# Optimization experiments

Measured on AMD Instinct MI355X. Metric: run time of the kernel, lower is better.

The kernel has to match this reference:

```python
import jax, jax.numpy as jnp
import numpy as np
from jax import lax

B, L = 2, 1024
D_MODEL, D_STATE, EXPAND, D_CONV = 1024, 16, 2, 4
D_INNER = EXPAND * D_MODEL            # 2048
DT_RANK = (D_MODEL + 15) // 16        # 64


def setup_inputs() -> dict:
    key = jax.random.key(0)
    ks = jax.random.split(key, 8)
    g = lambda k, shape, s=0.02: jax.random.normal(k, shape, dtype=jnp.float32) * s
    # Mamba-style A init: A = -exp(A_log), A_log = log(1..d_state) per channel
    A_log = jnp.log(jnp.broadcast_to(
        jnp.arange(1, D_STATE + 1, dtype=jnp.float32), (D_INNER, D_STATE)))
    return {
        "x": jax.random.normal(ks[0], (B, L, D_MODEL), dtype=jnp.float32),
        "W_in": g(ks[1], (D_MODEL, 2 * D_INNER)),
        "conv_w": g(ks[2], (D_INNER, D_CONV), 0.1),
        "conv_b": jnp.zeros((D_INNER,), jnp.float32),
        "W_x": g(ks[3], (D_INNER, DT_RANK + 2 * D_STATE)),
        "W_dt": g(ks[4], (DT_RANK, D_INNER)),
        "b_dt": g(ks[5], (D_INNER,), 0.1),
        "A_log": A_log,
        "D_skip": jnp.ones((D_INNER,), jnp.float32),
        "W_out": g(ks[6], (D_INNER, D_MODEL)),
    }


def reference(x, W_in, conv_w, conv_b, W_x, W_dt, b_dt, A_log, D_skip, W_out):
    # in_proj -> (u, z): [B, L, D_INNER] each
    xz = x @ W_in
    u, z = xz[..., :D_INNER], xz[..., D_INNER:]

    # causal depthwise conv1d, kernel D_CONV (small fixed loop over taps)
    up = jnp.pad(u, ((0, 0), (D_CONV - 1, 0), (0, 0)))
    u = sum(up[:, k:k + L, :] * conv_w[:, k] for k in range(D_CONV)) + conv_b
    u = jax.nn.silu(u)

    # input-dependent dt, B, C
    x_dbl = u @ W_x                                    # [B, L, dt_rank + 2N]
    dt = x_dbl[..., :DT_RANK]
    Bm = x_dbl[..., DT_RANK:DT_RANK + D_STATE]         # [B, L, N]
    Cm = x_dbl[..., DT_RANK + D_STATE:]                # [B, L, N]
    delta = jax.nn.softplus(dt @ W_dt + b_dt)          # [B, L, D]

    A = -jnp.exp(A_log)                                # [D, N]
    deltaA = jnp.exp(jnp.einsum('bld,dn->bldn', delta, A))   # [B, L, D, N]
    dBu = (delta * u)[..., None] * Bm[:, :, None, :]          # [B, L, D, N]

    def step(h, inp):
        dA_t, dBu_t, c_t = inp                         # [B,D,N],[B,D,N],[B,N]
        h = dA_t * h + dBu_t
        y_t = jnp.einsum('bdn,bn->bd', h, c_t)
        return h, y_t

    h0 = jnp.zeros((B, D_INNER, D_STATE), x.dtype)
    _, ys = lax.scan(step, h0,
                     (deltaA.transpose(1, 0, 2, 3),
                      dBu.transpose(1, 0, 2, 3),
                      Cm.transpose(1, 0, 2)))
    y = ys.transpose(1, 0, 2) + u * D_skip             # [B, L, D_INNER]
    y = y * jax.nn.silu(z)                             # gated output
    return y @ W_out                                   # [B, L, D_MODEL]
```

## Files before the change

kernel.cpp:

```cpp
#include <hip/hip_runtime.h>


typedef unsigned short u16;
typedef unsigned int   u32;

#define B_SZ 2
#define L_SZ 1024
#define DM   1024
#define DI   2048
#define DS   16
#define DTR  64
#define NXD  96
#define NCHUNK 32
#define CL   32
#define KSPLIT 8
#define KC     256

typedef __bf16 bf16x8 __attribute__((ext_vector_type(8)));
typedef float  f32x4  __attribute__((ext_vector_type(4)));

__device__ __forceinline__ u16 f2bf(float f) {
    u32 x = __float_as_uint(f);
    x += 0x7fffu + ((x >> 16) & 1u);
    return (u16)(x >> 16);
}
__device__ __forceinline__ float bf2f(u16 v) {
    return __uint_as_float(((u32)v) << 16);
}

__device__ __forceinline__ void gld_lds16(const u16* g, u16* l) {
    __builtin_amdgcn_global_load_lds(
        (const __attribute__((address_space(1))) u32*)g,
        (__attribute__((address_space(3))) u32*)l, 16, 0, 0);
}

__device__ __forceinline__ void wg_barrier() {
    __asm__ volatile("" ::: "memory");
    __builtin_amdgcn_s_barrier();
    __asm__ volatile("" ::: "memory");
}
#define WAIT_VM12() __builtin_amdgcn_s_waitcnt(0xF7C)
#define WAIT_VM9()  __builtin_amdgcn_s_waitcnt(0xF79)
#define WAIT_VM8()  __builtin_amdgcn_s_waitcnt(0xF78)
#define WAIT_VM6()  __builtin_amdgcn_s_waitcnt(0xF76)
#define WAIT_VM4()  __builtin_amdgcn_s_waitcnt(0xF74)
#define WAIT_VM3()  __builtin_amdgcn_s_waitcnt(0xF73)
#define WAIT_VM0()  __builtin_amdgcn_s_waitcnt(0xF70)

__global__ __launch_bounds__(256) void gemm128p(
    const u16* __restrict__ A, const u16* __restrict__ BT,
    float* __restrict__ Cf, u16* __restrict__ Cb,
    int M, int N, int K, int op)
{
    __shared__ u16 As[4][128 * 32];
    __shared__ u16 Bs[4][128 * 32];

    const int tid  = threadIdx.x;
    const int wave = tid >> 6;
    const int lane = tid & 63;
    const int q    = lane >> 4;
    const int r16  = lane & 15;
    const int wm   = (wave & 1) * 64;
    const int wn   = (wave >> 1) * 64;
    const int m0   = blockIdx.y * 128;
    const int n0   = blockIdx.x * 128;

    const u16* gA0 = A  + (size_t)(m0 + (tid >> 2))      * K + (tid & 3) * 8;
    const u16* gA1 = A  + (size_t)(m0 + 64 + (tid >> 2)) * K + (tid & 3) * 8;
    const u16* gB0 = BT + (size_t)(n0 + (tid >> 2))      * K + (tid & 3) * 8;
    const u16* gB1 = BT + (size_t)(n0 + 64 + (tid >> 2)) * K + (tid & 3) * 8;

    const int niter = K >> 5;
    const int pre = niter < 3 ? niter : 3;
    for (int p = 0; p < pre; ++p) {
        const int k0 = p * 32;
        gld_lds16(gA0 + k0, &As[p][tid * 8]);
        gld_lds16(gA1 + k0, &As[p][2048 + tid * 8]);
        gld_lds16(gB0 + k0, &Bs[p][tid * 8]);
        gld_lds16(gB1 + k0, &Bs[p][2048 + tid * 8]);
    }

    f32x4 acc[4][4];
#pragma unroll
    for (int s = 0; s < 4; ++s)
#pragma unroll
        for (int j = 0; j < 4; ++j) acc[s][j] = (f32x4){0.f, 0.f, 0.f, 0.f};

    for (int it = 0; it < niter; ++it) {
        if (it + 3 < niter) {
            const int k0 = (it + 3) * 32;
            const int bi = (it + 3) & 3;
            gld_lds16(gA0 + k0, &As[bi][tid * 8]);
            gld_lds16(gA1 + k0, &As[bi][2048 + tid * 8]);
            gld_lds16(gB0 + k0, &Bs[bi][tid * 8]);
            gld_lds16(gB1 + k0, &Bs[bi][2048 + tid * 8]);
            WAIT_VM12();
        } else if (it + 2 < niter) {
            WAIT_VM8();
        } else if (it + 1 < niter) {
            WAIT_VM4();
        } else {
            WAIT_VM0();
        }
        wg_barrier();

        const int cur = it & 3;
        bf16x8 af[4], bfr[4];
#pragma unroll
        for (int s = 0; s < 4; ++s)
            af[s] = *(const bf16x8*)(&As[cur][(wm + s * 16 + r16) * 32 + q * 8]);
#pragma unroll
        for (int j = 0; j < 4; ++j)
            bfr[j] = *(const bf16x8*)(&Bs[cur][(wn + j * 16 + r16) * 32 + q * 8]);
#pragma unroll
        for (int s = 0; s < 4; ++s)
#pragma unroll
            for (int j = 0; j < 4; ++j)
                acc[s][j] = __builtin_amdgcn_mfma_f32_16x16x32_bf16(
                    af[s], bfr[j], acc[s][j], 0, 0, 0);

        wg_barrier();
    }

#pragma unroll
    for (int s = 0; s < 4; ++s) {
        const int row0 = m0 + wm + s * 16 + q * 4;
#pragma unroll
        for (int j = 0; j < 4; ++j) {
            const int col = n0 + wn + j * 16 + r16;
            if (op == 2) {
#pragma unroll
                for (int i = 0; i < 4; ++i)
                    Cb[(size_t)(row0 + i) * N + col] = f2bf(acc[s][j][i]);
            } else {
#pragma unroll
                for (int i = 0; i < 4; ++i)
                    Cf[(size_t)(row0 + i) * N + col] = acc[s][j][i];
            }
        }
    }
}

__global__ __launch_bounds__(256) void gemm_out64(
    const u16* __restrict__ A, const u16* __restrict__ BT,
    float* __restrict__ C, int M, int N, int K)
{
    __shared__ u16 As[4][128 * 32];
    __shared__ u16 Bs[4][64 * 32];

    const int tid  = threadIdx.x;
    const int wave = tid >> 6;
    const int lane = tid & 63;
    const int q    = lane >> 4;
    const int r16  = lane & 15;
    const int wm   = (wave & 1) * 64;
    const int wn   = (wave >> 1) * 32;
    const int m0   = blockIdx.y * 128;
    const int n0   = blockIdx.x * 64;

    const u16* gA0 = A  + (size_t)(m0 + (tid >> 2))      * K + (tid & 3) * 8;
    const u16* gA1 = A  + (size_t)(m0 + 64 + (tid >> 2)) * K + (tid & 3) * 8;
    const u16* gB0 = BT + (size_t)(n0 + (tid >> 2))      * K + (tid & 3) * 8;

    const int niter = K >> 5;
    const int pre = niter < 3 ? niter : 3;
    for (int p = 0; p < pre; ++p) {
        const int k0 = p * 32;
        gld_lds16(gA0 + k0, &As[p][tid * 8]);
        gld_lds16(gA1 + k0, &As[p][2048 + tid * 8]);
        gld_lds16(gB0 + k0, &Bs[p][tid * 8]);
    }

    f32x4 acc[4][2];
#pragma unroll
    for (int s = 0; s < 4; ++s)
#pragma unroll
        for (int j = 0; j < 2; ++j) acc[s][j] = (f32x4){0.f, 0.f, 0.f, 0.f};

    for (int it = 0; it < niter; ++it) {
        if (it + 3 < niter) {
            const int k0 = (it + 3) * 32;
            const int bi = (it + 3) & 3;
            gld_lds16(gA0 + k0, &As[bi][tid * 8]);
            gld_lds16(gA1 + k0, &As[bi][2048 + tid * 8]);
            gld_lds16(gB0 + k0, &Bs[bi][tid * 8]);
            WAIT_VM9();
        } else if (it + 2 < niter) {
            WAIT_VM6();
        } else if (it + 1 < niter) {
            WAIT_VM3();
        } else {
            WAIT_VM0();
        }
        wg_barrier();

        const int cur = it & 3;
        bf16x8 af[4], bfr[2];
#pragma unroll
        for (int s = 0; s < 4; ++s)
            af[s] = *(const bf16x8*)(&As[cur][(wm + s * 16 + r16) * 32 + q * 8]);
#pragma unroll
        for (int j = 0; j < 2; ++j)
            bfr[j] = *(const bf16x8*)(&Bs[cur][(wn + j * 16 + r16) * 32 + q * 8]);
#pragma unroll
        for (int s = 0; s < 4; ++s)
#pragma unroll
            for (int j = 0; j < 2; ++j)
                acc[s][j] = __builtin_amdgcn_mfma_f32_16x16x32_bf16(
                    af[s], bfr[j], acc[s][j], 0, 0, 0);

        wg_barrier();
    }

#pragma unroll
    for (int s = 0; s < 4; ++s) {
        const int row0 = m0 + wm + s * 16 + q * 4;
#pragma unroll
        for (int j = 0; j < 2; ++j) {
            const int col = n0 + wn + j * 16 + r16;
#pragma unroll
            for (int i = 0; i < 4; ++i)
                C[(size_t)(row0 + i) * N + col] = acc[s][j][i];
        }
    }
}

__global__ __launch_bounds__(256) void gemm_skinny_atomic(
    const u16* __restrict__ A, const u16* __restrict__ BT,
    float* xdbl, int M, int N, int K)
{
    constexpr int LDT = 40;
    __shared__ u16 As[128 * LDT];
    __shared__ u16 Bs[64 * LDT];

    const int tid  = threadIdx.x;
    const int wave = tid >> 6;
    const int lane = tid & 63;
    const int q    = lane >> 4;
    const int r16  = lane & 15;
    const int m0   = blockIdx.y * 128;
    const int n0   = blockIdx.x * 64;
    const int kcs  = blockIdx.z * KC;
    const int sr   = tid >> 2;
    const int ss   = (tid & 3) * 8;

    f32x4 acc[2][4];
#pragma unroll
    for (int s = 0; s < 2; ++s)
#pragma unroll
        for (int j = 0; j < 4; ++j) acc[s][j] = (f32x4){0.f, 0.f, 0.f, 0.f};

    const int bcol  = n0 + sr;
    const int bcolc = bcol < N ? bcol : N - 1;

    constexpr int NIT = KC / 32;
    uint4 a0 = *(const uint4*)(A + (size_t)(m0 + sr)      * K + kcs + ss);
    uint4 a1 = *(const uint4*)(A + (size_t)(m0 + 64 + sr) * K + kcs + ss);
    uint4 bv = *(const uint4*)(BT + (size_t)bcolc * K + kcs + ss);

    for (int it = 0; it < NIT; ++it) {
        wg_barrier();
        *(uint4*)(As + sr * LDT + ss)        = a0;
        *(uint4*)(As + (64 + sr) * LDT + ss) = a1;
        *(uint4*)(Bs + sr * LDT + ss)        = bv;
        const int kn = (it + 1 < NIT) ? (kcs + (it + 1) * 32) : kcs;
        a0 = *(const uint4*)(A + (size_t)(m0 + sr)      * K + kn + ss);
        a1 = *(const uint4*)(A + (size_t)(m0 + 64 + sr) * K + kn + ss);
        bv = *(const uint4*)(BT + (size_t)bcolc * K + kn + ss);
        __builtin_amdgcn_s_waitcnt(0xF70 | 0x0000);
        __builtin_amdgcn_s_waitcnt(0x070F);
        wg_barrier();

        bf16x8 af[2], bfr[4];
#pragma unroll
        for (int s = 0; s < 2; ++s)
            af[s] = *(const bf16x8*)(As + (wave * 32 + s * 16 + r16) * LDT + q * 8);
#pragma unroll
        for (int j = 0; j < 4; ++j)
            bfr[j] = *(const bf16x8*)(Bs + (j * 16 + r16) * LDT + q * 8);
#pragma unroll
        for (int s = 0; s < 2; ++s)
#pragma unroll
            for (int j = 0; j < 4; ++j)
                acc[s][j] = __builtin_amdgcn_mfma_f32_16x16x32_bf16(
                    af[s], bfr[j], acc[s][j], 0, 0, 0);
    }

#pragma unroll
    for (int s = 0; s < 2; ++s) {
        const int row0 = m0 + wave * 32 + s * 16 + q * 4;
#pragma unroll
        for (int j = 0; j < 4; ++j) {
            const int col = n0 + j * 16 + r16;
            if (col < N) {
#pragma unroll
                for (int i = 0; i < 4; ++i)
                    atomicAdd(&xdbl[(size_t)(row0 + i) * N + col], acc[s][j][i]);
            }
        }
    }
}

__global__ __launch_bounds__(256) void gemm_delta(
    const float* __restrict__ xdbl, const u16* __restrict__ BT,
    const float* __restrict__ bias, float* __restrict__ dlt)
{
    constexpr int LDT = 40;
    __shared__ u16 As[128 * LDT];
    __shared__ u16 Bs[128 * LDT];

    const int tid  = threadIdx.x;
    const int wave = tid >> 6;
    const int lane = tid & 63;
    const int q    = lane >> 4;
    const int r16  = lane & 15;
    const int wm   = (wave & 1) * 64;
    const int wn   = (wave >> 1) * 64;
    const int m0   = blockIdx.y * 128;
    const int n0   = blockIdx.x * 128;
    const int sr   = tid >> 2;
    const int ss   = (tid & 3) * 8;

    f32x4 acc[4][4];
#pragma unroll
    for (int s = 0; s < 4; ++s)
#pragma unroll
        for (int j = 0; j < 4; ++j) acc[s][j] = (f32x4){0.f, 0.f, 0.f, 0.f};

    for (int k0 = 0; k0 < DTR; k0 += 32) {
        __syncthreads();
        f32x4 f0 = *(const f32x4*)(xdbl + (size_t)(m0 + sr) * NXD + k0 + ss);
        f32x4 f1 = *(const f32x4*)(xdbl + (size_t)(m0 + sr) * NXD + k0 + ss + 4);
        f32x4 f2 = *(const f32x4*)(xdbl + (size_t)(m0 + 64 + sr) * NXD + k0 + ss);
        f32x4 f3 = *(const f32x4*)(xdbl + (size_t)(m0 + 64 + sr) * NXD + k0 + ss + 4);
        uint4 bv0 = *(const uint4*)(BT + (size_t)(n0 + sr)      * DTR + k0 + ss);
        uint4 bv1 = *(const uint4*)(BT + (size_t)(n0 + 64 + sr) * DTR + k0 + ss);
        u16* pa0 = As + sr * LDT + ss;
        u16* pa1 = As + (64 + sr) * LDT + ss;
#pragma unroll
        for (int i = 0; i < 4; ++i) { pa0[i] = f2bf(f0[i]); pa0[4 + i] = f2bf(f1[i]); }
#pragma unroll
        for (int i = 0; i < 4; ++i) { pa1[i] = f2bf(f2[i]); pa1[4 + i] = f2bf(f3[i]); }
        *(uint4*)(Bs + sr * LDT + ss)        = bv0;
        *(uint4*)(Bs + (64 + sr) * LDT + ss) = bv1;
        __syncthreads();

        bf16x8 af[4], bfr[4];
#pragma unroll
        for (int s = 0; s < 4; ++s)
            af[s] = *(const bf16x8*)(As + (wm + s * 16 + r16) * LDT + q * 8);
#pragma unroll
        for (int j = 0; j < 4; ++j)
            bfr[j] = *(const bf16x8*)(Bs + (wn + j * 16 + r16) * LDT + q * 8);
#pragma unroll
        for (int s = 0; s < 4; ++s)
#pragma unroll
            for (int j = 0; j < 4; ++j)
                acc[s][j] = __builtin_amdgcn_mfma_f32_16x16x32_bf16(
                    af[s], bfr[j], acc[s][j], 0, 0, 0);
    }

#pragma unroll
    for (int s = 0; s < 4; ++s) {
        const int row0 = m0 + wm + s * 16 + q * 4;
#pragma unroll
        for (int j = 0; j < 4; ++j) {
            const int col = n0 + wn + j * 16 + r16;
            const float bv = bias[col];
#pragma unroll
            for (int i = 0; i < 4; ++i) {
                float v = acc[s][j][i] + bv;
                v = (v > 20.f) ? v : log1pf(__expf(v));
                dlt[(size_t)(row0 + i) * DI + col] = v;
            }
        }
    }
}

__device__ __forceinline__ void tr_tile(
    const float* __restrict__ in, u16* __restrict__ out,
    int R, int C, int tr, int tc, int tid, float (*t)[33])
{
    const int tx = tid & 31, ty = tid >> 5;
    const int r0 = tr * 32, c0 = tc * 32;
#pragma unroll
    for (int i = 0; i < 4; ++i) {
        int r = r0 + ty + i * 8, c = c0 + tx;
        if (r < R && c < C) t[ty + i * 8][tx] = in[(size_t)r * C + c];
    }
    __syncthreads();
#pragma unroll
    for (int i = 0; i < 4; ++i) {
        int oR = c0 + ty + i * 8, oC = r0 + tx;
        if (oR < C && oC < R) out[(size_t)oR * R + oC] = f2bf(t[tx][ty + i * 8]);
    }
}

__global__ __launch_bounds__(256) void prep_kernel(
    const float* __restrict__ x,     u16* __restrict__ xbf,
    const float* __restrict__ W_in,  u16* __restrict__ winT,
    const float* __restrict__ W_out, u16* __restrict__ woutT,
    const float* __restrict__ W_x,   u16* __restrict__ wxT,
    const float* __restrict__ W_dt,  u16* __restrict__ wdtT,
    float* __restrict__ xdbl)
{
    __shared__ float t[32][33];
    const int id  = blockIdx.x;
    const int tid = threadIdx.x;
    if (id < 4096) {
        tr_tile(W_in, winT, 1024, 4096, id >> 7, id & 127, tid, t);
    } else if (id < 6144) {
        int i2 = id - 4096;
        tr_tile(W_out, woutT, 2048, 1024, i2 >> 5, i2 & 31, tid, t);
    } else if (id < 6336) {
        int i3 = id - 6144;
        tr_tile(W_x, wxT, 2048, 96, i3 / 3, i3 % 3, tid, t);
    } else if (id < 6464) {
        int i4 = id - 6336;
        tr_tile(W_dt, wdtT, 64, 2048, i4 >> 6, i4 & 63, tid, t);
    } else if (id < 14656) {
        int i = (id - 6464) * 256 + tid;
        xbf[i] = f2bf(x[i]);
    } else {
        f32x4 z = (f32x4){0.f, 0.f, 0.f, 0.f};
        ((f32x4*)xdbl)[(size_t)(id - 14656) * 256 + tid] = z;
    }
}

__global__ __launch_bounds__(256) void conv_silu_kernel(
    const u16* __restrict__ xzbf, const float* __restrict__ cw,
    const float* __restrict__ cb, u16* __restrict__ ucbf)
{
    const int idx = blockIdx.x * 256 + threadIdx.x;
    const int d   = idx & (DI - 1);
    const int pos = idx >> 11;
    const int l   = pos & (L_SZ - 1);
    float s = cb[d];
#pragma unroll
    for (int k = 0; k < 4; ++k) {
        int ls = l + k - 3;
        if (ls >= 0)
            s = fmaf(bf2f(xzbf[(size_t)(pos + k - 3) * (2 * DI) + d]), cw[d * 4 + k], s);
    }
    float v = s / (1.f + __expf(-s));
    ucbf[idx] = f2bf(v);
}

__global__ __launch_bounds__(256) void scan_pass1(
    const float* __restrict__ delta, const u16* __restrict__ ucbf,
    const float* __restrict__ xdbl, const float* __restrict__ A_log,
    float* __restrict__ hbuf, float* __restrict__ pbuf)
{
    const int c = blockIdx.x;
    const int d = blockIdx.y * 256 + threadIdx.x;
    const int b = blockIdx.z;
    float Av[16], h[16], P[16];
#pragma unroll
    for (int n = 0; n < 16; ++n) {
        Av[n] = -__expf(A_log[d * 16 + n]);
        h[n] = 0.f; P[n] = 1.f;
    }
    const int rowbase = b * L_SZ + c * CL;
    for (int i = 0; i < CL; ++i) {
        const int row = rowbase + i;
        float dlt = delta[(size_t)row * DI + d];
        float uu  = bf2f(ucbf[(size_t)row * DI + d]);
        float du  = dlt * uu;
        const float* xr = xdbl + (size_t)row * NXD;
#pragma unroll
        for (int n = 0; n < 16; ++n) {
            float e = __expf(dlt * Av[n]);
            P[n] *= e;
            h[n] = fmaf(e, h[n], du * xr[DTR + n]);
        }
    }
    size_t base = ((size_t)((b * NCHUNK + c) * DI + d)) * 16;
#pragma unroll
    for (int n = 0; n < 16; ++n) { hbuf[base + n] = h[n]; pbuf[base + n] = P[n]; }
}

__global__ __launch_bounds__(256) void scan_pass2(
    float* __restrict__ hbuf, const float* __restrict__ pbuf)
{
    const int j = blockIdx.x * 256 + threadIdx.x;
    const int b = blockIdx.y;
    float h0 = 0.f;
    for (int cc = 0; cc < NCHUNK; ++cc) {
        size_t o = ((size_t)(b * NCHUNK + cc)) * (DI * 16) + j;
        float hl = hbuf[o];
        float Pl = pbuf[o];
        hbuf[o] = h0;
        h0 = fmaf(Pl, h0, hl);
    }
}

__global__ __launch_bounds__(256) void scan_pass3(
    const float* __restrict__ delta, const u16* __restrict__ ucbf,
    const float* __restrict__ xdbl, const float* __restrict__ A_log,
    const float* __restrict__ hbuf, const u16* __restrict__ xzbf,
    const float* __restrict__ Dskip, u16* __restrict__ ybf)
{
    const int c = blockIdx.x;
    const int d = blockIdx.y * 256 + threadIdx.x;
    const int b = blockIdx.z;
    float Av[16], h[16];
    size_t base = ((size_t)((b * NCHUNK + c) * DI + d)) * 16;
#pragma unroll
    for (int n = 0; n < 16; ++n) {
        Av[n] = -__expf(A_log[d * 16 + n]);
        h[n]  = hbuf[base + n];
    }
    const float Dk = Dskip[d];
    const int rowbase = b * L_SZ + c * CL;
    for (int i = 0; i < CL; ++i) {
        const int row = rowbase + i;
        float dlt = delta[(size_t)row * DI + d];
        float uu  = bf2f(ucbf[(size_t)row * DI + d]);
        float du  = dlt * uu;
        const float* xr = xdbl + (size_t)row * NXD;
        float y = 0.f;
#pragma unroll
        for (int n = 0; n < 16; ++n) {
            float e = __expf(dlt * Av[n]);
            h[n] = fmaf(e, h[n], du * xr[DTR + n]);
            y = fmaf(h[n], xr[DTR + DS + n], y);
        }
        float zz = bf2f(xzbf[(size_t)row * (2 * DI) + DI + d]);
        float yv = fmaf(uu, Dk, y) * (zz / (1.f + __expf(-zz)));
        ybf[(size_t)row * DI + d] = f2bf(yv);
    }
}

constexpr size_t OFF_DELTA   = 0;
constexpr size_t OFF_XDBL    = OFF_DELTA + 4194304;
constexpr size_t OFF_HBUF    = OFF_XDBL  + 196608;
constexpr size_t OFF_PBUF    = OFF_HBUF  + 2097152;
constexpr size_t OFF_F32_END = OFF_PBUF  + 2097152;
constexpr size_t SOFF_XBF   = 0;
constexpr size_t SOFF_WINT  = SOFF_XBF   + 2097152;
constexpr size_t SOFF_XZBF  = SOFF_WINT  + 4194304;
constexpr size_t SOFF_UCBF  = SOFF_XZBF  + 8388608;
constexpr size_t SOFF_WXT   = SOFF_UCBF  + 4194304;
constexpr size_t SOFF_WDTT  = SOFF_WXT   + 196608;
constexpr size_t SOFF_WOUTT = SOFF_WDTT  + 131072;
constexpr size_t SOFF_YBF   = SOFF_WOUTT + 2097152;

extern "C" void kernel_launch(void* const* d_in, const int* in_sizes, int n_in,
                              void* d_out, int out_size, void* d_ws, size_t ws_size,
                              hipStream_t stream)
{
    const float* x     = (const float*)d_in[0];
    const float* W_in  = (const float*)d_in[1];
    const float* cw    = (const float*)d_in[2];
    const float* cb    = (const float*)d_in[3];
    const float* W_x   = (const float*)d_in[4];
    const float* W_dt  = (const float*)d_in[5];
    const float* b_dt  = (const float*)d_in[6];
    const float* A_log = (const float*)d_in[7];
    const float* Dsk   = (const float*)d_in[8];
    const float* W_out = (const float*)d_in[9];
    float* out = (float*)d_out;

    float* wsf   = (float*)d_ws;
    float* dlt   = wsf + OFF_DELTA;
    float* xdbl  = wsf + OFF_XDBL;
    float* hbuf  = wsf + OFF_HBUF;
    float* pbuf  = wsf + OFF_PBUF;
    u16* sb    = (u16*)(wsf + OFF_F32_END);
    u16* xbf   = sb + SOFF_XBF;
    u16* winT  = sb + SOFF_WINT;
    u16* xzbf  = sb + SOFF_XZBF;
    u16* ucbf  = sb + SOFF_UCBF;
    u16* wxT   = sb + SOFF_WXT;
    u16* wdtT  = sb + SOFF_WDTT;
    u16* woutT = sb + SOFF_WOUTT;
    u16* ybf   = sb + SOFF_YBF;

    prep_kernel<<<14848, 256, 0, stream>>>(x, xbf, W_in, winT, W_out, woutT,
                                           W_x, wxT, W_dt, wdtT, xdbl);

    gemm128p<<<dim3(32, 16), 256, 0, stream>>>(
        xbf, winT, nullptr, xzbf, 2048, 4096, 1024, 2);

    conv_silu_kernel<<<(B_SZ * L_SZ * DI) / 256, 256, 0, stream>>>(xzbf, cw, cb, ucbf);

    gemm_skinny_atomic<<<dim3(2, 16, KSPLIT), 256, 0, stream>>>(
        ucbf, wxT, xdbl, 2048, NXD, 2048);

    gemm_delta<<<dim3(16, 16), 256, 0, stream>>>(xdbl, wdtT, b_dt, dlt);

    scan_pass1<<<dim3(NCHUNK, DI / 256, B_SZ), 256, 0, stream>>>(dlt, ucbf, xdbl, A_log, hbuf, pbuf);
    scan_pass2<<<dim3(DI * 16 / 256, B_SZ), 256, 0, stream>>>(hbuf, pbuf);
    scan_pass3<<<dim3(NCHUNK, DI / 256, B_SZ), 256, 0, stream>>>(dlt, ucbf, xdbl, A_log, hbuf, xzbf, Dsk, ybf);

    gemm_out64<<<dim3(16, 16), 256, 0, stream>>>(ybf, woutT, out, 2048, 1024, 2048);
}
```

Measured before the change: 261.8 us.

## Fuse conv, x_proj, delta GEMM and scan passes into cooperative persistent kernel

After: 801.2 us. 3.06x slower.

```diff
diff --git a/kernel.cpp b/kernel.cpp
--- a/kernel.cpp
+++ b/kernel.cpp
@@ -1,4 +1,7 @@
 #include <hip/hip_runtime.h>
+#include <hip/hip_cooperative_groups.h>
+
+namespace cg = cooperative_groups;
 
 
 typedef unsigned short u16;
@@ -267,7 +270,6 @@
         a0 = *(const uint4*)(A + (size_t)(m0 + sr)      * K + kn + ss);
         a1 = *(const uint4*)(A + (size_t)(m0 + 64 + sr) * K + kn + ss);
         bv = *(const uint4*)(BT + (size_t)bcolc * K + kn + ss);
-        __builtin_amdgcn_s_waitcnt(0xF70 | 0x0000);
         __builtin_amdgcn_s_waitcnt(0x070F);
         wg_barrier();
 
@@ -373,6 +375,369 @@
                 v = (v > 20.f) ? v : log1pf(__expf(v));
                 dlt[(size_t)(row0 + i) * DI + col] = v;
             }
+        }
+    }
+}
+
+__global__ __launch_bounds__(256) void conv_silu_kernel(
+    const u16* __restrict__ xzbf, const float* __restrict__ cw,
+    const float* __restrict__ cb, u16* __restrict__ ucbf)
+{
+    const int idx = blockIdx.x * 256 + threadIdx.x;
+    const int d   = idx & (DI - 1);
+    const int pos = idx >> 11;
+    const int l   = pos & (L_SZ - 1);
+    float s = cb[d];
+#pragma unroll
+    for (int k = 0; k < 4; ++k) {
+        int ls = l + k - 3;
+        if (ls >= 0)
+            s = fmaf(bf2f(xzbf[(size_t)(pos + k - 3) * (2 * DI) + d]), cw[d * 4 + k], s);
+    }
+    float v = s / (1.f + __expf(-s));
+    ucbf[idx] = f2bf(v);
+}
+
+__global__ __launch_bounds__(256) void scan_pass1(
+    const float* __restrict__ delta, const u16* __restrict__ ucbf,
+    const float* __restrict__ xdbl, const float* __restrict__ A_log,
+    float* __restrict__ hbuf, float* __restrict__ pbuf)
+{
+    const int c = blockIdx.x;
+    const int d = blockIdx.y * 256 + threadIdx.x;
+    const int b = blockIdx.z;
+    float Av[16], h[16], P[16];
+#pragma unroll
+    for (int n = 0; n < 16; ++n) {
+        Av[n] = -__expf(A_log[d * 16 + n]);
+        h[n] = 0.f; P[n] = 1.f;
+    }
+    const int rowbase = b * L_SZ + c * CL;
+    for (int i = 0; i < CL; ++i) {
+        const int row = rowbase + i;
+        float dlt = delta[(size_t)row * DI + d];
+        float uu  = bf2f(ucbf[(size_t)row * DI + d]);
+        float du  = dlt * uu;
+        const float* xr = xdbl + (size_t)row * NXD;
+#pragma unroll
+        for (int n = 0; n < 16; ++n) {
+            float e = __expf(dlt * Av[n]);
+            P[n] *= e;
+            h[n] = fmaf(e, h[n], du * xr[DTR + n]);
+        }
+    }
+    size_t base = ((size_t)((b * NCHUNK + c) * DI + d)) * 16;
+#pragma unroll
+    for (int n = 0; n < 16; ++n) { hbuf[base + n] = h[n]; pbuf[base + n] = P[n]; }
+}
+
+__global__ __launch_bounds__(256) void scan_pass2(
+    float* __restrict__ hbuf, const float* __restrict__ pbuf)
+{
+    const int j = blockIdx.x * 256 + threadIdx.x;
+    const int b = blockIdx.y;
+    float h0 = 0.f;
+    for (int cc = 0; cc < NCHUNK; ++cc) {
+        size_t o = ((size_t)(b * NCHUNK + cc)) * (DI * 16) + j;
+        float hl = hbuf[o];
+        float Pl = pbuf[o];
+        hbuf[o] = h0;
+        h0 = fmaf(Pl, h0, hl);
+    }
+}
+
+__global__ __launch_bounds__(256) void scan_pass3(
+    const float* __restrict__ delta, const u16* __restrict__ ucbf,
+    const float* __restrict__ xdbl, const float* __restrict__ A_log,
+    const float* __restrict__ hbuf, const u16* __restrict__ xzbf,
+    const float* __restrict__ Dskip, u16* __restrict__ ybf)
+{
+    const int c = blockIdx.x;
+    const int d = blockIdx.y * 256 + threadIdx.x;
+    const int b = blockIdx.z;
+    float Av[16], h[16];
+    size_t base = ((size_t)((b * NCHUNK + c) * DI + d)) * 16;
+#pragma unroll
+    for (int n = 0; n < 16; ++n) {
+        Av[n] = -__expf(A_log[d * 16 + n]);
+        h[n]  = hbuf[base + n];
+    }
+    const float Dk = Dskip[d];
+    const int rowbase = b * L_SZ + c * CL;
+    for (int i = 0; i < CL; ++i) {
+        const int row = rowbase + i;
+        float dlt = delta[(size_t)row * DI + d];
+        float uu  = bf2f(ucbf[(size_t)row * DI + d]);
+        float du  = dlt * uu;
+        const float* xr = xdbl + (size_t)row * NXD;
+        float y = 0.f;
+#pragma unroll
+        for (int n = 0; n < 16; ++n) {
+            float e = __expf(dlt * Av[n]);
+            h[n] = fmaf(e, h[n], du * xr[DTR + n]);
+            y = fmaf(h[n], xr[DTR + DS + n], y);
+        }
+        float zz = bf2f(xzbf[(size_t)row * (2 * DI) + DI + d]);
+        float yv = fmaf(uu, Dk, y) * (zz / (1.f + __expf(-zz)));
+        ybf[(size_t)row * DI + d] = f2bf(yv);
+    }
+}
+
+#define MEGA_BLOCKS 512
+#define MEGA_THREADS_TOTAL (MEGA_BLOCKS * 256)
+
+__global__ __launch_bounds__(256, 2) void mega_kernel(
+    const u16* __restrict__ xzbf, const float* __restrict__ cw,
+    const float* __restrict__ cb, u16* __restrict__ ucbf,
+    const u16* __restrict__ wxT, float* __restrict__ xdbl,
+    const u16* __restrict__ wdtT, const float* __restrict__ b_dt,
+    float* __restrict__ dlt, const float* __restrict__ A_log,
+    float* __restrict__ hbuf, float* __restrict__ pbuf,
+    const float* __restrict__ Dsk, u16* __restrict__ ybf)
+{
+    constexpr int LDT = 40;
+    __shared__ u16 sA[128 * LDT];
+    __shared__ u16 sB[64 * LDT];
+
+    cg::grid_group grid = cg::this_grid();
+
+    const int blk = blockIdx.x;
+    const int tid = threadIdx.x;
+    const int wave = tid >> 6;
+    const int lane = tid & 63;
+    const int q    = lane >> 4;
+    const int r16  = lane & 15;
+
+    {
+        for (int idx = blk * 256 + tid; idx < B_SZ * L_SZ * DI;
+             idx += MEGA_THREADS_TOTAL) {
+            const int d   = idx & (DI - 1);
+            const int pos = idx >> 11;
+            const int l   = pos & (L_SZ - 1);
+            float s = cb[d];
+#pragma unroll
+            for (int k = 0; k < 4; ++k) {
+                int ls = l + k - 3;
+                if (ls >= 0)
+                    s = fmaf(bf2f(xzbf[(size_t)(pos + k - 3) * (2 * DI) + d]),
+                             cw[d * 4 + k], s);
+            }
+            float v = s / (1.f + __expf(-s));
+            ucbf[idx] = f2bf(v);
+        }
+    }
+    __threadfence();
+    grid.sync();
+
+    if (blk < 2 * 16 * KSPLIT) {
+        const int n0  = (blk & 1) * 64;
+        const int m0  = ((blk >> 1) & 15) * 128;
+        const int kcs = (blk >> 5) * KC;
+        const int sr  = tid >> 2;
+        const int ss  = (tid & 3) * 8;
+        const int K   = DI;
+        const int N   = NXD;
+
+        f32x4 acc[2][4];
+#pragma unroll
+        for (int s = 0; s < 2; ++s)
+#pragma unroll
+            for (int j = 0; j < 4; ++j) acc[s][j] = (f32x4){0.f, 0.f, 0.f, 0.f};
+
+        const int bcol  = n0 + sr;
+        const int bcolc = bcol < N ? bcol : N - 1;
+
+        constexpr int NIT = KC / 32;
+        uint4 a0 = *(const uint4*)(ucbf + (size_t)(m0 + sr)      * K + kcs + ss);
+        uint4 a1 = *(const uint4*)(ucbf + (size_t)(m0 + 64 + sr) * K + kcs + ss);
+        uint4 bv = *(const uint4*)(wxT + (size_t)bcolc * K + kcs + ss);
+
+        for (int it = 0; it < NIT; ++it) {
+            wg_barrier();
+            *(uint4*)(sA + sr * LDT + ss)        = a0;
+            *(uint4*)(sA + (64 + sr) * LDT + ss) = a1;
+            *(uint4*)(sB + sr * LDT + ss)        = bv;
+            const int kn = (it + 1 < NIT) ? (kcs + (it + 1) * 32) : kcs;
+            a0 = *(const uint4*)(ucbf + (size_t)(m0 + sr)      * K + kn + ss);
+            a1 = *(const uint4*)(ucbf + (size_t)(m0 + 64 + sr) * K + kn + ss);
+            bv = *(const uint4*)(wxT + (size_t)bcolc * K + kn + ss);
+            __builtin_amdgcn_s_waitcnt(0x070F);
+            wg_barrier();
+
+            bf16x8 af[2], bfr[4];
+#pragma unroll
+            for (int s = 0; s < 2; ++s)
+                af[s] = *(const bf16x8*)(sA + (wave * 32 + s * 16 + r16) * LDT + q * 8);
+#pragma unroll
+            for (int j = 0; j < 4; ++j)
+                bfr[j] = *(const bf16x8*)(sB + (j * 16 + r16) * LDT + q * 8);
+#pragma unroll
+            for (int s = 0; s < 2; ++s)
+#pragma unroll
+                for (int j = 0; j < 4; ++j)
+                    acc[s][j] = __builtin_amdgcn_mfma_f32_16x16x32_bf16(
+                        af[s], bfr[j], acc[s][j], 0, 0, 0);
+        }
+
+#pragma unroll
+        for (int s = 0; s < 2; ++s) {
+            const int row0 = m0 + wave * 32 + s * 16 + q * 4;
+#pragma unroll
+            for (int j = 0; j < 4; ++j) {
+                const int col = n0 + j * 16 + r16;
+                if (col < N) {
+#pragma unroll
+                    for (int i = 0; i < 4; ++i)
+                        atomicAdd(&xdbl[(size_t)(row0 + i) * N + col], acc[s][j][i]);
+                }
+            }
+        }
+    }
+    __threadfence();
+    grid.sync();
+
+    {
+        const int n0 = (blk & 31) * 64;
+        const int m0 = (blk >> 5) * 128;
+        const int wm = (wave & 1) * 64;
+        const int wn = (wave >> 1) * 32;
+        const int sr = tid >> 2;
+        const int ss = (tid & 3) * 8;
+
+        f32x4 acc[4][2];
+#pragma unroll
+        for (int s = 0; s < 4; ++s)
+#pragma unroll
+            for (int j = 0; j < 2; ++j) acc[s][j] = (f32x4){0.f, 0.f, 0.f, 0.f};
+
+        for (int k0 = 0; k0 < DTR; k0 += 32) {
+            __syncthreads();
+            f32x4 f0 = *(const f32x4*)(xdbl + (size_t)(m0 + sr) * NXD + k0 + ss);
+            f32x4 f1 = *(const f32x4*)(xdbl + (size_t)(m0 + sr) * NXD + k0 + ss + 4);
+            f32x4 f2 = *(const f32x4*)(xdbl + (size_t)(m0 + 64 + sr) * NXD + k0 + ss);
+            f32x4 f3 = *(const f32x4*)(xdbl + (size_t)(m0 + 64 + sr) * NXD + k0 + ss + 4);
+            uint4 bv0 = *(const uint4*)(wdtT + (size_t)(n0 + sr) * DTR + k0 + ss);
+            u16* pa0 = sA + sr * LDT + ss;
+            u16* pa1 = sA + (64 + sr) * LDT + ss;
+#pragma unroll
+            for (int i = 0; i < 4; ++i) { pa0[i] = f2bf(f0[i]); pa0[4 + i] = f2bf(f1[i]); }
+#pragma unroll
+            for (int i = 0; i < 4; ++i) { pa1[i] = f2bf(f2[i]); pa1[4 + i] = f2bf(f3[i]); }
+            *(uint4*)(sB + sr * LDT + ss) = bv0;
+            __syncthreads();
+
+            bf16x8 af[4], bfr[2];
+#pragma unroll
+            for (int s = 0; s < 4; ++s)
+                af[s] = *(const bf16x8*)(sA + (wm + s * 16 + r16) * LDT + q * 8);
+#pragma unroll
+            for (int j = 0; j < 2; ++j)
+                bfr[j] = *(const bf16x8*)(sB + (wn + j * 16 + r16) * LDT + q * 8);
+#pragma unroll
+            for (int s = 0; s < 4; ++s)
+#pragma unroll
+                for (int j = 0; j < 2; ++j)
+                    acc[s][j] = __builtin_amdgcn_mfma_f32_16x16x32_bf16(
+                        af[s], bfr[j], acc[s][j], 0, 0, 0);
+        }
+
+#pragma unroll
+        for (int s = 0; s < 4; ++s) {
+            const int row0 = m0 + wm + s * 16 + q * 4;
+#pragma unroll
+            for (int j = 0; j < 2; ++j) {
+                const int col = n0 + wn + j * 16 + r16;
+                const float bv = b_dt[col];
+#pragma unroll
+                for (int i = 0; i < 4; ++i) {
+                    float v = acc[s][j][i] + bv;
+                    v = (v > 20.f) ? v : log1pf(__expf(v));
+                    dlt[(size_t)(row0 + i) * DI + col] = v;
+                }
+            }
+        }
+    }
+    __threadfence();
+    grid.sync();
+
+    {
+        const int c = blk & 31;
+        const int d = ((blk >> 5) & 7) * 256 + tid;
+        const int b = blk >> 8;
+        float Av[16], h[16], P[16];
+#pragma unroll
+        for (int n = 0; n < 16; ++n) {
+            Av[n] = -__expf(A_log[d * 16 + n]);
+            h[n] = 0.f; P[n] = 1.f;
+        }
+        const int rowbase = b * L_SZ + c * CL;
+        for (int i = 0; i < CL; ++i) {
+            const int row = rowbase + i;
+            float dl = dlt[(size_t)row * DI + d];
+            float uu = bf2f(ucbf[(size_t)row * DI + d]);
+            float du = dl * uu;
+            const float* xr = xdbl + (size_t)row * NXD;
+#pragma unroll
+            for (int n = 0; n < 16; ++n) {
+                float e = __expf(dl * Av[n]);
+                P[n] *= e;
+                h[n] = fmaf(e, h[n], du * xr[DTR + n]);
+            }
+        }
+        size_t base = ((size_t)((b * NCHUNK + c) * DI + d)) * 16;
+#pragma unroll
+        for (int n = 0; n < 16; ++n) { hbuf[base + n] = h[n]; pbuf[base + n] = P[n]; }
+    }
+    __threadfence();
+    grid.sync();
+
+    {
+        const int idx = blk * 256 + tid;
+        if (idx < B_SZ * DI * 16) {
+            const int b = idx >> 15;
+            const int j = idx & (DI * 16 - 1);
+            float h0 = 0.f;
+            for (int cc = 0; cc < NCHUNK; ++cc) {
+                size_t o = ((size_t)(b * NCHUNK + cc)) * (DI * 16) + j;
+                float hl = hbuf[o];
+                float Pl = pbuf[o];
+                hbuf[o] = h0;
+                h0 = fmaf(Pl, h0, hl);
+            }
+        }
+    }
+    __threadfence();
+    grid.sync();
+
+    {
+        const int c = blk & 31;
+        const int d = ((blk >> 5) & 7) * 256 + tid;
+        const int b = blk >> 8;
+        float Av[16], h[16];
+        size_t base = ((size_t)((b * NCHUNK + c) * DI + d)) * 16;
+#pragma unroll
+        for (int n = 0; n < 16; ++n) {
+            Av[n] = -__expf(A_log[d * 16 + n]);
+            h[n]  = hbuf[base + n];
+        }
+        const float Dk = Dsk[d];
+        const int rowbase = b * L_SZ + c * CL;
+        for (int i = 0; i < CL; ++i) {
+            const int row = rowbase + i;
+            float dl = dlt[(size_t)row * DI + d];
+            float uu = bf2f(ucbf[(size_t)row * DI + d]);
+            float du = dl * uu;
+            const float* xr = xdbl + (size_t)row * NXD;
+            float y = 0.f;
+#pragma unroll
+            for (int n = 0; n < 16; ++n) {
+                float e = __expf(dl * Av[n]);
+                h[n] = fmaf(e, h[n], du * xr[DTR + n]);
+                y = fmaf(h[n], xr[DTR + DS + n], y);
+            }
+            float zz = bf2f(xzbf[(size_t)row * (2 * DI) + DI + d]);
+            float yv = fmaf(uu, Dk, y) * (zz / (1.f + __expf(-zz)));
+            ybf[(size_t)row * DI + d] = f2bf(yv);
         }
     }
 }
@@ -427,110 +792,6 @@
     }
 }
 
-__global__ __launch_bounds__(256) void conv_silu_kernel(
-    const u16* __restrict__ xzbf, const float* __restrict__ cw,
-    const float* __restrict__ cb, u16* __restrict__ ucbf)
-{
-    const int idx = blockIdx.x * 256 + threadIdx.x;
-    const int d   = idx & (DI - 1);
-    const int pos = idx >> 11;
-    const int l   = pos & (L_SZ - 1);
-    float s = cb[d];
-#pragma unroll
-    for (int k = 0; k < 4; ++k) {
-        int ls = l + k - 3;
-        if (ls >= 0)
-            s = fmaf(bf2f(xzbf[(size_t)(pos + k - 3) * (2 * DI) + d]), cw[d * 4 + k], s);
-    }
-    float v = s / (1.f + __expf(-s));
-    ucbf[idx] = f2bf(v);
-}
-
-__global__ __launch_bounds__(256) void scan_pass1(
-    const float* __restrict__ delta, const u16* __restrict__ ucbf,
-    const float* __restrict__ xdbl, const float* __restrict__ A_log,
-    float* __restrict__ hbuf, float* __restrict__ pbuf)
-{
-    const int c = blockIdx.x;
-    const int d = blockIdx.y * 256 + threadIdx.x;
-    const int b = blockIdx.z;
-    float Av[16], h[16], P[16];
-#pragma unroll
-    for (int n = 0; n < 16; ++n) {
-        Av[n] = -__expf(A_log[d * 16 + n]);
-        h[n] = 0.f; P[n] = 1.f;
-    }
-    const int rowbase = b * L_SZ + c * CL;
-    for (int i = 0; i < CL; ++i) {
-        const int row = rowbase + i;
-        float dlt = delta[(size_t)row * DI + d];
-        float uu  = bf2f(ucbf[(size_t)row * DI + d]);
-        float du  = dlt * uu;
-        const float* xr = xdbl + (size_t)row * NXD;
-#pragma unroll
-        for (int n = 0; n < 16; ++n) {
-            float e = __expf(dlt * Av[n]);
-            P[n] *= e;
-            h[n] = fmaf(e, h[n], du * xr[DTR + n]);
-        }
-    }
-    size_t base = ((size_t)((b * NCHUNK + c) * DI + d)) * 16;
-#pragma unroll
-    for (int n = 0; n < 16; ++n) { hbuf[base + n] = h[n]; pbuf[base + n] = P[n]; }
-}
-
-__global__ __launch_bounds__(256) void scan_pass2(
-    float* __restrict__ hbuf, const float* __restrict__ pbuf)
-{
-    const int j = blockIdx.x * 256 + threadIdx.x;
-    const int b = blockIdx.y;
-    float h0 = 0.f;
-    for (int cc = 0; cc < NCHUNK; ++cc) {
-        size_t o = ((size_t)(b * NCHUNK + cc)) * (DI * 16) + j;
-        float hl = hbuf[o];
-        float Pl = pbuf[o];
-        hbuf[o] = h0;
-        h0 = fmaf(Pl, h0, hl);
-    }
-}
-
-__global__ __launch_bounds__(256) void scan_pass3(
-    const float* __restrict__ delta, const u16* __restrict__ ucbf,
-    const float* __restrict__ xdbl, const float* __restrict__ A_log,
-    const float* __restrict__ hbuf, const u16* __restrict__ xzbf,
-    const float* __restrict__ Dskip, u16* __restrict__ ybf)
-{
-    const int c = blockIdx.x;
-    const int d = blockIdx.y * 256 + threadIdx.x;
-    const int b = blockIdx.z;
-    float Av[16], h[16];
-    size_t base = ((size_t)((b * NCHUNK + c) * DI + d)) * 16;
-#pragma unroll
-    for (int n = 0; n < 16; ++n) {
-        Av[n] = -__expf(A_log[d * 16 + n]);
-        h[n]  = hbuf[base + n];
-    }
-    const float Dk = Dskip[d];
-    const int rowbase = b * L_SZ + c * CL;
-    for (int i = 0; i < CL; ++i) {
-        const int row = rowbase + i;
-        float dlt = delta[(size_t)row * DI + d];
-        float uu  = bf2f(ucbf[(size_t)row * DI + d]);
-        float du  = dlt * uu;
-        const float* xr = xdbl + (size_t)row * NXD;
-        float y = 0.f;
-#pragma unroll
-        for (int n = 0; n < 16; ++n) {
-            float e = __expf(dlt * Av[n]);
-            h[n] = fmaf(e, h[n], du * xr[DTR + n]);
-            y = fmaf(h[n], xr[DTR + DS + n], y);
-        }
-        float zz = bf2f(xzbf[(size_t)row * (2 * DI) + DI + d]);
-        float yv = fmaf(uu, Dk, y) * (zz / (1.f + __expf(-zz)));
-        ybf[(size_t)row * DI + d] = f2bf(yv);
-    }
-}
-
 constexpr size_t OFF_DELTA   = 0;
 constexpr size_t OFF_XDBL    = OFF_DELTA + 4194304;
 constexpr size_t OFF_HBUF    = OFF_XDBL  + 196608;
@@ -582,16 +843,29 @@
     gemm128p<<<dim3(32, 16), 256, 0, stream>>>(
         xbf, winT, nullptr, xzbf, 2048, 4096, 1024, 2);
 
-    conv_silu_kernel<<<(B_SZ * L_SZ * DI) / 256, 256, 0, stream>>>(xzbf, cw, cb, ucbf);
-
-    gemm_skinny_atomic<<<dim3(2, 16, KSPLIT), 256, 0, stream>>>(
-        ucbf, wxT, xdbl, 2048, NXD, 2048);
-
-    gemm_delta<<<dim3(16, 16), 256, 0, stream>>>(xdbl, wdtT, b_dt, dlt);
-
-    scan_pass1<<<dim3(NCHUNK, DI / 256, B_SZ), 256, 0, stream>>>(dlt, ucbf, xdbl, A_log, hbuf, pbuf);
-    scan_pass2<<<dim3(DI * 16 / 256, B_SZ), 256, 0, stream>>>(hbuf, pbuf);
-    scan_pass3<<<dim3(NCHUNK, DI / 256, B_SZ), 256, 0, stream>>>(dlt, ucbf, xdbl, A_log, hbuf, xzbf, Dsk, ybf);
+    {
+        void* kargs[] = {
+            (void*)&xzbf, (void*)&cw, (void*)&cb, (void*)&ucbf,
+            (void*)&wxT, (void*)&xdbl, (void*)&wdtT, (void*)&b_dt,
+            (void*)&dlt, (void*)&A_log, (void*)&hbuf, (void*)&pbuf,
+            (void*)&Dsk, (void*)&ybf
+        };
+        hipError_t ce = hipLaunchCooperativeKernel(
+            (const void*)mega_kernel, dim3(MEGA_BLOCKS), dim3(256),
+            kargs, 0, stream);
+        if (ce != hipSuccess) {
+            conv_silu_kernel<<<(B_SZ * L_SZ * DI) / 256, 256, 0, stream>>>(
+                xzbf, cw, cb, ucbf);
+            gemm_skinny_atomic<<<dim3(2, 16, KSPLIT), 256, 0, stream>>>(
+                ucbf, wxT, xdbl, 2048, NXD, 2048);
+            gemm_delta<<<dim3(16, 16), 256, 0, stream>>>(xdbl, wdtT, b_dt, dlt);
+            scan_pass1<<<dim3(NCHUNK, DI / 256, B_SZ), 256, 0, stream>>>(
+                dlt, ucbf, xdbl, A_log, hbuf, pbuf);
+            scan_pass2<<<dim3(DI * 16 / 256, B_SZ), 256, 0, stream>>>(hbuf, pbuf);
+            scan_pass3<<<dim3(NCHUNK, DI / 256, B_SZ), 256, 0, stream>>>(
+                dlt, ucbf, xdbl, A_log, hbuf, xzbf, Dsk, ybf);
+        }
+    }
 
     gemm_out64<<<dim3(16, 16), 256, 0, stream>>>(ybf, woutT, out, 2048, 1024, 2048);
 }
```

## Fuse causal conv and SiLU into the skinny x_proj GEMM prologue

Applied to the files above, without the earlier changes.

New measurement: 249.1 us. 1.05x faster.

```diff
diff --git a/kernel.cpp b/kernel.cpp
--- a/kernel.cpp
+++ b/kernel.cpp
@@ -18,6 +18,7 @@
 
 typedef __bf16 bf16x8 __attribute__((ext_vector_type(8)));
 typedef float  f32x4  __attribute__((ext_vector_type(4)));
+typedef u16    u16x8  __attribute__((ext_vector_type(8)));
 
 __device__ __forceinline__ u16 f2bf(float f) {
     u32 x = __float_as_uint(f);
@@ -46,6 +47,7 @@
 #define WAIT_VM4()  __builtin_amdgcn_s_waitcnt(0xF74)
 #define WAIT_VM3()  __builtin_amdgcn_s_waitcnt(0xF73)
 #define WAIT_VM0()  __builtin_amdgcn_s_waitcnt(0xF70)
+#define WAIT_LGKM0() __builtin_amdgcn_s_waitcnt(0xC07F)
 
 __global__ __launch_bounds__(256) void gemm128p(
     const u16* __restrict__ A, const u16* __restrict__ BT,
@@ -225,13 +227,18 @@
     }
 }
 
-__global__ __launch_bounds__(256) void gemm_skinny_atomic(
-    const u16* __restrict__ A, const u16* __restrict__ BT,
-    float* xdbl, int M, int N, int K)
+__global__ __launch_bounds__(256) void gemm_skinny_conv(
+    const u16* __restrict__ xz, const u16* __restrict__ BT,
+    const float* __restrict__ cw, const float* __restrict__ cb,
+    u16* __restrict__ ucbf, float* xdbl)
 {
     constexpr int LDT = 40;
+    constexpr int XLD = 40;
     __shared__ u16 As[128 * LDT];
     __shared__ u16 Bs[64 * LDT];
+    __shared__ u16 sxz[131 * XLD];
+    __shared__ float cwS[1024];
+    __shared__ float cbS[256];
 
     const int tid  = threadIdx.x;
     const int wave = tid >> 6;
@@ -243,6 +250,12 @@
     const int kcs  = blockIdx.z * KC;
     const int sr   = tid >> 2;
     const int ss   = (tid & 3) * 8;
+    constexpr int XROW = 2 * DI;
+    const bool halo_ok = (m0 & (L_SZ - 1)) != 0;
+
+    *(f32x4*)(cwS + tid * 4) = *(const f32x4*)(cw + (size_t)kcs * 4 + tid * 4);
+    if (tid < 64)
+        *(f32x4*)(cbS + tid * 4) = *(const f32x4*)(cb + kcs + tid * 4);
 
     f32x4 acc[2][4];
 #pragma unroll
@@ -251,24 +264,74 @@
         for (int j = 0; j < 4; ++j) acc[s][j] = (f32x4){0.f, 0.f, 0.f, 0.f};
 
     const int bcol  = n0 + sr;
-    const int bcolc = bcol < N ? bcol : N - 1;
+    const int bcolc = bcol < NXD ? bcol : NXD - 1;
 
     constexpr int NIT = KC / 32;
-    uint4 a0 = *(const uint4*)(A + (size_t)(m0 + sr)      * K + kcs + ss);
-    uint4 a1 = *(const uint4*)(A + (size_t)(m0 + 64 + sr) * K + kcs + ss);
-    uint4 bv = *(const uint4*)(BT + (size_t)bcolc * K + kcs + ss);
+    uint4 xa0 = *(const uint4*)(xz + (size_t)(m0 + sr)      * XROW + kcs + ss);
+    uint4 xa1 = *(const uint4*)(xz + (size_t)(m0 + 64 + sr) * XROW + kcs + ss);
+    uint4 bv  = *(const uint4*)(BT + (size_t)bcolc * DI + kcs + ss);
+    uint4 hv  = (uint4){0, 0, 0, 0};
+    const int hr  = tid >> 2;
+    const int hss = (tid & 3) * 8;
+    if (tid < 12 && halo_ok)
+        hv = *(const uint4*)(xz + (size_t)(m0 - 3 + hr) * XROW + kcs + hss);
 
     for (int it = 0; it < NIT; ++it) {
+        const int k0 = kcs + it * 32;
         wg_barrier();
-        *(uint4*)(As + sr * LDT + ss)        = a0;
-        *(uint4*)(As + (64 + sr) * LDT + ss) = a1;
+        *(uint4*)(sxz + (3 + sr) * XLD + ss)  = xa0;
+        *(uint4*)(sxz + (67 + sr) * XLD + ss) = xa1;
+        if (tid < 12) *(uint4*)(sxz + hr * XLD + hss) = hv;
+        WAIT_LGKM0();
+        wg_barrier();
+
+        if (it + 1 < NIT) {
+            const int kn = k0 + 32;
+            xa0 = *(const uint4*)(xz + (size_t)(m0 + sr)      * XROW + kn + ss);
+            xa1 = *(const uint4*)(xz + (size_t)(m0 + 64 + sr) * XROW + kn + ss);
+            if (tid < 12 && halo_ok)
+                hv = *(const uint4*)(xz + (size_t)(m0 - 3 + hr) * XROW + kn + hss);
+        }
+
+        f32x4 cwv[8];
+#pragma unroll
+        for (int i = 0; i < 8; ++i)
+            cwv[i] = *(const f32x4*)(cwS + (it * 32 + ss + i) * 4);
+        float s0[8], s1[8];
+#pragma unroll
+        for (int i = 0; i < 8; ++i) { s0[i] = cbS[it * 32 + ss + i]; s1[i] = s0[i]; }
+#pragma unroll
+        for (int j = 0; j < 4; ++j) {
+            u16x8 t0 = *(const u16x8*)(sxz + (sr + j) * XLD + ss);
+            u16x8 t1 = *(const u16x8*)(sxz + (64 + sr + j) * XLD + ss);
+#pragma unroll
+            for (int i = 0; i < 8; ++i) {
+                s0[i] = fmaf(bf2f(t0[i]), cwv[i][j], s0[i]);
+                s1[i] = fmaf(bf2f(t1[i]), cwv[i][j], s1[i]);
+            }
+        }
+        u32 p0[4], p1[4];
+#pragma unroll
+        for (int i = 0; i < 4; ++i) {
+            float v0a = s0[2*i],   v0b = s0[2*i+1];
+            float v1a = s1[2*i],   v1b = s1[2*i+1];
+            v0a = v0a / (1.f + __expf(-v0a));  v0b = v0b / (1.f + __expf(-v0b));
+            v1a = v1a / (1.f + __expf(-v1a));  v1b = v1b / (1.f + __expf(-v1b));
+            p0[i] = (u32)f2bf(v0a) | ((u32)f2bf(v0b) << 16);
+            p1[i] = (u32)f2bf(v1a) | ((u32)f2bf(v1b) << 16);
+        }
+        uint4 ua = (uint4){p0[0], p0[1], p0[2], p0[3]};
+        uint4 ub = (uint4){p1[0], p1[1], p1[2], p1[3]};
+        *(uint4*)(As + sr * LDT + ss)        = ua;
+        *(uint4*)(As + (64 + sr) * LDT + ss) = ub;
         *(uint4*)(Bs + sr * LDT + ss)        = bv;
-        const int kn = (it + 1 < NIT) ? (kcs + (it + 1) * 32) : kcs;
-        a0 = *(const uint4*)(A + (size_t)(m0 + sr)      * K + kn + ss);
-        a1 = *(const uint4*)(A + (size_t)(m0 + 64 + sr) * K + kn + ss);
-        bv = *(const uint4*)(BT + (size_t)bcolc * K + kn + ss);
-        __builtin_amdgcn_s_waitcnt(0xF70 | 0x0000);
-        __builtin_amdgcn_s_waitcnt(0x070F);
+        if (n0 == 0) {
+            *(uint4*)(ucbf + (size_t)(m0 + sr)      * DI + k0 + ss) = ua;
+            *(uint4*)(ucbf + (size_t)(m0 + 64 + sr) * DI + k0 + ss) = ub;
+        }
+        if (it + 1 < NIT)
+            bv = *(const uint4*)(BT + (size_t)bcolc * DI + k0 + 32 + ss);
+        WAIT_LGKM0();
         wg_barrier();
 
         bf16x8 af[2], bfr[4];
@@ -292,10 +355,10 @@
 #pragma unroll
         for (int j = 0; j < 4; ++j) {
             const int col = n0 + j * 16 + r16;
-            if (col < N) {
+            if (col < NXD) {
 #pragma unroll
                 for (int i = 0; i < 4; ++i)
-                    atomicAdd(&xdbl[(size_t)(row0 + i) * N + col], acc[s][j][i]);
+                    atomicAdd(&xdbl[(size_t)(row0 + i) * NXD + col], acc[s][j][i]);
             }
         }
     }
@@ -427,25 +490,6 @@
     }
 }
 
-__global__ __launch_bounds__(256) void conv_silu_kernel(
-    const u16* __restrict__ xzbf, const float* __restrict__ cw,
-    const float* __restrict__ cb, u16* __restrict__ ucbf)
-{
-    const int idx = blockIdx.x * 256 + threadIdx.x;
-    const int d   = idx & (DI - 1);
-    const int pos = idx >> 11;
-    const int l   = pos & (L_SZ - 1);
-    float s = cb[d];
-#pragma unroll
-    for (int k = 0; k < 4; ++k) {
-        int ls = l + k - 3;
-        if (ls >= 0)
-            s = fmaf(bf2f(xzbf[(size_t)(pos + k - 3) * (2 * DI) + d]), cw[d * 4 + k], s);
-    }
-    float v = s / (1.f + __expf(-s));
-    ucbf[idx] = f2bf(v);
-}
-
 __global__ __launch_bounds__(256) void scan_pass1(
     const float* __restrict__ delta, const u16* __restrict__ ucbf,
     const float* __restrict__ xdbl, const float* __restrict__ A_log,
@@ -582,10 +626,8 @@
     gemm128p<<<dim3(32, 16), 256, 0, stream>>>(
         xbf, winT, nullptr, xzbf, 2048, 4096, 1024, 2);
 
-    conv_silu_kernel<<<(B_SZ * L_SZ * DI) / 256, 256, 0, stream>>>(xzbf, cw, cb, ucbf);
-
-    gemm_skinny_atomic<<<dim3(2, 16, KSPLIT), 256, 0, stream>>>(
-        ucbf, wxT, xdbl, 2048, NXD, 2048);
+    gemm_skinny_conv<<<dim3(2, 16, KSPLIT), 256, 0, stream>>>(
+        xzbf, wxT, cw, cb, ucbf, xdbl);
 
     gemm_delta<<<dim3(16, 16), 256, 0, stream>>>(xdbl, wdtT, b_dt, dlt);
 
```
